# Performance work log

Hardware: AMD Instinct MI355X
Metric: run time of the kernel (lower is better)

## Reference

```python
import jax, jax.numpy as jnp
import numpy as np

N, D, B, P, T = 2048, 64, 64, 16384, 262144
EPS = 1e-6        # const.eps in the original repo
LAST_TIME = 1.0   # init_time = 0


def setup_inputs() -> dict:
    key = jax.random.key(0)
    k = jax.random.split(key, 8)
    x0 = jax.random.normal(k[0], (N, D), dtype=jnp.float32)
    v = 0.1 * jax.random.normal(k[1], (B, N, D), dtype=jnp.float32)
    beta = jax.random.normal(k[2], (N,), dtype=jnp.float32)
    bins_rwidth = jax.random.normal(k[3], (B,), dtype=jnp.float32)
    # distinct node pairs (i != j) to avoid degenerate zero-distance pairs
    i = jax.random.randint(k[4], (P,), 0, N, dtype=jnp.int32)
    off = jax.random.randint(k[5], (P,), 1, N, dtype=jnp.int32)
    node_pairs = jnp.stack([i, (i + off) % N], axis=0)  # [2, P]
    event_times = jax.random.uniform(k[6], (T,), dtype=jnp.float32) * LAST_TIME
    event_pair_idx = jax.random.randint(k[7], (T,), 0, P, dtype=jnp.int32)
    return {"x0": x0, "v": v, "beta": beta, "bins_rwidth": bins_rwidth,
            "event_times": event_times, "node_pairs": node_pairs,
            "event_pair_idx": event_pair_idx}


def reference(x0, v, beta, bins_rwidth, event_times, node_pairs, event_pair_idx):
    # bin bounds: softmax(relative widths) -> cumsum over the timeline
    bounds = jnp.concatenate([jnp.zeros((1,), x0.dtype),
                              jnp.cumsum(jax.nn.softmax(bins_rwidth)) * LAST_TIME])  # [B+1]
    widths = bounds[1:] - bounds[:-1]          # [B]
    inner = bounds[1:-1]                       # bucketize boundaries

    i, j = node_pairs[0], node_pairs[1]
    dx0 = x0[i] - x0[j]                        # [P, D]
    dv = v[:, i, :] - v[:, j, :]               # [B, P, D]
    # cumulative displacement at each bin boundary
    cum = jnp.concatenate([jnp.zeros((1, dx0.shape[0], dx0.shape[1]), dx0.dtype),
                           jnp.cumsum(dv * widths[:, None, None], axis=0)], axis=0)  # [B+1, P, D]
    beta_sum = beta[i] + beta[j]               # [P]

    # ---- intensity integral over the bin bounds (closed form per bin) ----
    idx_b = jnp.searchsorted(inner, bounds, side='right')          # torch.bucketize right=True
    rem_b = bounds - bounds[idx_b]
    xt_b = dx0[None] + cum[idx_b] + dv[idx_b] * rem_b[:, None, None]  # [B+1, P, D]
    norm_b = jnp.linalg.norm(xt_b, axis=2)                         # [B+1, P]
    numer = norm_b * jnp.exp(beta_sum[None, :] - norm_b)
    dot1 = jnp.sum(xt_b[1:] * dv, axis=2)                          # [B, P]
    dot0 = jnp.sum(xt_b[:-1] * dv, axis=2)
    integral = jnp.sum(numer[1:] / (dot1 + EPS) - numer[:-1] / (dot0 + EPS))

    # ---- ragged event log-intensities (flattened: events -> pair ids) ----
    idx_e = jnp.searchsorted(inner, event_times, side='right')     # [T]
    rem_e = event_times - bounds[idx_e]
    pid = event_pair_idx
    xt_e = dx0[pid] + cum[idx_e, pid] + dv[idx_e, pid] * rem_e[:, None]  # [T, D]
    dist_e = jnp.linalg.norm(xt_e, axis=1)
    non_integral = jnp.sum(beta_sum[pid] - dist_e)

    # NLL = -(-integral + non_integral)
    return integral - non_integral
```

## Files before the change

### kernel.cpp

```cpp
#include <hip/hip_runtime.h>

#define NN 2048
#define DD 64
#define BB 64
#define PP 16384
#define TT 262144
#define EPSF 1e-6f
#define SS ((size_t)NN * DD)


typedef unsigned uv2 __attribute__((ext_vector_type(2)));
using bf16x8 = __attribute__((ext_vector_type(8))) short;
using f32x4v = __attribute__((ext_vector_type(4))) float;

template <int CTRL, int RM = 0xF, bool BC = true>
__device__ __forceinline__ float dpp_add(float x) {
    int y = __builtin_amdgcn_update_dpp(0, __float_as_int(x), CTRL, RM, 0xF, BC);
    return x + __int_as_float(y);
}

template <int PAT>
__device__ __forceinline__ float swz_add(float x) {
    return x + __int_as_float(__builtin_amdgcn_ds_swizzle(__float_as_int(x), PAT));
}

__device__ __forceinline__ float xor16_add(float x) {
#if __has_builtin(__builtin_amdgcn_permlane16_swap)
    uv2 r = __builtin_amdgcn_permlane16_swap(__float_as_uint(x), __float_as_uint(x),
                                             false, false);
    return __uint_as_float(r.x) + __uint_as_float(r.y);
#else
    return swz_add<0x401F>(x);
#endif
}
__device__ __forceinline__ float xor32_add(float x) {
#if __has_builtin(__builtin_amdgcn_permlane32_swap)
    uv2 r = __builtin_amdgcn_permlane32_swap(__float_as_uint(x), __float_as_uint(x),
                                             false, false);
    return __uint_as_float(r.x) + __uint_as_float(r.y);
#else
    return x + __shfl_xor(x, 32, 64);
#endif
}

__device__ __forceinline__ float reduce1(float a) {
    a = dpp_add<0xB1>(a);
    a = dpp_add<0x4E>(a);
    a = dpp_add<0x141>(a);
    a = swz_add<0x201F>(a);
    a = xor16_add(a);
    a = xor32_add(a);
    return a;
}

__device__ __forceinline__ float incl_scan(float x) {
    x = dpp_add<0x111>(x);
    x = dpp_add<0x112>(x);
    x = dpp_add<0x114>(x);
    x = dpp_add<0x118>(x);
    x = dpp_add<0x142, 0xA, false>(x);
    x = dpp_add<0x143, 0xC, false>(x);
    return x;
}

__device__ __forceinline__ unsigned short f2bf(float f) {
    unsigned u = __float_as_uint(f);
    unsigned r = (u + 0x7FFFu + ((u >> 16) & 1u)) >> 16;
    return (unsigned short)r;
}
__device__ __forceinline__ float bf_lo(unsigned u) { return __uint_as_float(u << 16); }
__device__ __forceinline__ float bf_hi(unsigned u) { return __uint_as_float(u & 0xFFFF0000u); }

__device__ __forceinline__ unsigned cvt_pk_bf(float lo, float hi) {
    unsigned r;
    asm("v_cvt_pk_bf16_f32 %0, %1, %2" : "=v"(r) : "v"(lo), "v"(hi));
    return r;
}
__device__ __forceinline__ float bpermf(float v, int srclane) {
    return __int_as_float(__builtin_amdgcn_ds_bpermute(srclane << 2, __float_as_int(v)));
}

__global__ void k_bounds(const float* __restrict__ brw, float* __restrict__ bounds,
                         float* __restrict__ widths, float* __restrict__ innerPad,
                         int* __restrict__ cnt, double* __restrict__ acc) {
    if (blockIdx.x != 0) {
        int t = (blockIdx.x - 1) * 64 + threadIdx.x;
#pragma unroll
        for (int k = 0; k < 4; k++) cnt[t * 4 + k] = 0;
        if (blockIdx.x == 1 && threadIdx.x == 0) acc[0] = 0.0;
        return;
    }
    int lane = threadIdx.x;
    float w = brw[lane];
    float m = w;
#pragma unroll
    for (int s = 32; s >= 1; s >>= 1) m = fmaxf(m, __shfl_xor(m, s, 64));
    float e = expf(w - m);
    float tot = e;
#pragma unroll
    for (int s = 32; s >= 1; s >>= 1) tot += __shfl_xor(tot, s, 64);
    float sm = e / tot;
    float c = sm;
#pragma unroll
    for (int off = 1; off < 64; off <<= 1) {
        float t = __shfl_up(c, off, 64);
        if (lane >= off) c += t;
    }
    float cexcl = __shfl_up(c, 1, 64);
    if (lane == 0) cexcl = 0.f;
    if (lane == 0) bounds[0] = 0.f;
    bounds[lane + 1] = c;
    widths[lane] = c - cexcl;
    innerPad[lane] = (lane == 63) ? 3.4e38f : c;
}

__global__ __launch_bounds__(256) void k_convert(const float* __restrict__ v,
                                                 unsigned* __restrict__ vh32) {
    int wid = threadIdx.x >> 6, lane = threadIdx.x & 63;
    int n = blockIdx.x * 4 + wid;
    int sub = lane >> 5;
    int dp = (lane & 31) * 2;
    unsigned* __restrict__ dst = vh32 + ((size_t)n * BB * DD) / 2;
#pragma unroll
    for (int c = 0; c < 32; c++) {
        int b = c * 2 + sub;
        float2 f = *(const float2*)(v + (size_t)b * SS + (size_t)n * DD + dp);
        unsigned pk = (unsigned)f2bf(f.x) | ((unsigned)f2bf(f.y) << 16);
        dst[(b * DD + dp) / 2] = pk;
    }
}

__global__ void k_hist2(const int* __restrict__ pairs, int* __restrict__ cnt) {
    int t = blockIdx.x * 256 + threadIdx.x;
    atomicAdd(&cnt[pairs[t]], 1);
}

__global__ __launch_bounds__(1024) void k_scan2(const int* __restrict__ cnt,
                                                int* __restrict__ cursor) {
    __shared__ int waveTot[16];
    __shared__ int waveOff[16];
    int tid = threadIdx.x;
    int a = cnt[tid * 2], b = cnt[tid * 2 + 1];
    int s = a + b;
    int lane = tid & 63, wid = tid >> 6;
    int incl = s;
#pragma unroll
    for (int off = 1; off < 64; off <<= 1) {
        int t2 = __shfl_up(incl, off, 64);
        if (lane >= off) incl += t2;
    }
    if (lane == 63) waveTot[wid] = incl;
    __syncthreads();
    if (tid == 0) {
        int r = 0;
        for (int w = 0; w < 16; w++) { waveOff[w] = r; r += waveTot[w]; }
    }
    __syncthreads();
    int run = waveOff[wid] + (incl - s);
    cursor[tid * 2] = run;
    cursor[tid * 2 + 1] = run + a;
}

__global__ void k_scatter2(const int* __restrict__ pairs, int* __restrict__ cursor,
                           int* __restrict__ perm) {
    int t = blockIdx.x * 256 + threadIdx.x;
    int pos = atomicAdd(&cursor[pairs[t]], 1);
    perm[pos] = t;
}

__global__ __launch_bounds__(256, 2) void k_pairs(
    const float* __restrict__ x0, const uint4* __restrict__ vh4,
    const float* __restrict__ beta, const int* __restrict__ pairs,
    const int* __restrict__ perm, const float* __restrict__ widths,
    float4* __restrict__ table, double* __restrict__ acc_out) {
    __shared__ double bacc[4];
    const int wid = threadIdx.x >> 6;
    const int lane = threadIdx.x & 63;
    const int bid = blockIdx.x;
    const int vb = ((bid & 7) << 7) | (bid >> 3);
    const int pbase = (vb * 4 + wid) * 4;

    int pk[4], ik[4], jk[4];
    float bs[4];
#pragma unroll
    for (int k = 0; k < 4; k++) pk[k] = perm[pbase + k];
#pragma unroll
    for (int k = 0; k < 4; k++) {
        ik[k] = pairs[pk[k]];
        jk[k] = pairs[PP + pk[k]];
    }
#pragma unroll
    for (int k = 0; k < 4; k++) bs[k] = beta[ik[k]] + beta[jk[k]];

    float wv[4][4];
#pragma unroll
    for (int tm = 0; tm < 4; tm++)
#pragma unroll
        for (int r = 0; r < 4; r++)
            wv[tm][r] = widths[16 * tm + (lane >> 4) * 4 + r];
    const float wl = widths[lane];
    const int laneterm = (lane & 15) * 8 + (lane >> 4);
    const int nl = lane & 15;
    const int mb = (lane >> 4) * 4;

    uint4 ra[8], rb[8];
    float xiv, xjv;

#define ISSUE(k_)                                                            \
    {                                                                        \
        const uint4* Vi = vh4 + (size_t)ik[k_] * 512 + laneterm;             \
        const uint4* Vj = vh4 + (size_t)jk[k_] * 512 + laneterm;             \
        _Pragma("unroll") for (int t = 0; t < 4; t++) {                      \
            ra[t * 2 + 0] = Vi[t * 128];                                     \
            ra[t * 2 + 1] = Vi[t * 128 + 4];                                 \
            rb[t * 2 + 0] = Vj[t * 128];                                     \
            rb[t * 2 + 1] = Vj[t * 128 + 4];                                 \
        }                                                                    \
        xiv = x0[ik[k_] * DD + lane];                                        \
        xjv = x0[jk[k_] * DD + lane];                                        \
    }

    ISSUE(0)

    double accd = 0.0;

#pragma unroll
    for (int k = 0; k < 4; k++) {
        const float bsum = bs[k];
        float dx0 = xiv - xjv;
        float n2_0 = reduce1(dx0 * dx0);
        float rr0 = __builtin_amdgcn_sqrtf(n2_0);
        float numer0 = rr0 * __expf(bsum - rr0);

        bf16x8 F[8];
#pragma unroll
        for (int f = 0; f < 8; f++) {
            uint4 q;
            q.x = cvt_pk_bf(bf_lo(ra[f].x) - bf_lo(rb[f].x), bf_hi(ra[f].x) - bf_hi(rb[f].x));
            q.y = cvt_pk_bf(bf_lo(ra[f].y) - bf_lo(rb[f].y), bf_hi(ra[f].y) - bf_hi(rb[f].y));
            q.z = cvt_pk_bf(bf_lo(ra[f].z) - bf_lo(rb[f].z), bf_hi(ra[f].z) - bf_hi(rb[f].z));
            q.w = cvt_pk_bf(bf_lo(ra[f].w) - bf_lo(rb[f].w), bf_hi(ra[f].w) - bf_hi(rb[f].w));
            union { uint4 u; bf16x8 s; } cv;
            cv.u = q;
            F[f] = cv.s;
        }

        if (k < 3) {
            if (k == 0) ISSUE(1)
            if (k == 1) ISSUE(2)
            if (k == 2) ISSUE(3)
        }

        bf16x8 AX[2];
#pragma unroll
        for (int kb = 0; kb < 2; kb++) {
            unsigned u[4];
#pragma unroll
            for (int c2 = 0; c2 < 4; c2++) {
                int k0 = kb * 32 + ((lane >> 4) << 3) + c2 * 2;
                u[c2] = cvt_pk_bf(bpermf(dx0, k0), bpermf(dx0, k0 + 1));
            }
            uint4 q;
            bool z = (lane & 15) != 0;
            q.x = z ? 0u : u[0]; q.y = z ? 0u : u[1];
            q.z = z ? 0u : u[2]; q.w = z ? 0u : u[3];
            union { uint4 uu; bf16x8 s; } cv;
            cv.uu = q;
            AX[kb] = cv.s;
        }

        f32x4v g00 = {0.f, 0.f, 0.f, 0.f}, g01 = g00, g02 = g00, g03 = g00;
        f32x4v g11 = g00, g12 = g00, g13 = g00, g22 = g00, g23 = g00, g33 = g00;
#define GMM(acc, ta, tb)                                                                       \
    acc = __builtin_amdgcn_mfma_f32_16x16x32_bf16(F[(ta)*2 + 0], F[(tb)*2 + 0], acc, 0, 0, 0); \
    acc = __builtin_amdgcn_mfma_f32_16x16x32_bf16(F[(ta)*2 + 1], F[(tb)*2 + 1], acc, 0, 0, 0);
        GMM(g00, 0, 0) GMM(g01, 0, 1) GMM(g02, 0, 2) GMM(g03, 0, 3)
        GMM(g11, 1, 1) GMM(g12, 1, 2) GMM(g13, 1, 3)
        GMM(g22, 2, 2) GMM(g23, 2, 3) GMM(g33, 3, 3)
#undef GMM
        float c00, c01, c02, c03;
        {
            f32x4v ca = {0.f, 0.f, 0.f, 0.f};
#define CMM(tb)                                                                        \
    ca = __builtin_amdgcn_mfma_f32_16x16x32_bf16(AX[0], F[(tb)*2 + 0], ca, 0, 0, 0);  \
    ca = __builtin_amdgcn_mfma_f32_16x16x32_bf16(AX[1], F[(tb)*2 + 1], ca, 0, 0, 0);
            CMM(0) c00 = ca[0]; ca = {0.f, 0.f, 0.f, 0.f};
            CMM(1) c01 = ca[0]; ca = {0.f, 0.f, 0.f, 0.f};
            CMM(2) c02 = ca[0]; ca = {0.f, 0.f, 0.f, 0.f};
            CMM(3) c03 = ca[0];
#undef CMM
        }

        float c0v;
        {
            float b0 = bpermf(c00, lane & 15);
            float b1 = bpermf(c01, lane & 15);
            float b2 = bpermf(c02, lane & 15);
            float b3 = bpermf(c03, lane & 15);
            int g = lane >> 4;
            c0v = (g == 0) ? b0 : (g == 1) ? b1 : (g == 2) ? b2 : b3;
        }

        float Sv = 0.f, qv = 0.f;
#define OFFT(gt, t_) (wv[t_][0] * gt[0] + wv[t_][1] * gt[1] + wv[t_][2] * gt[2] + wv[t_][3] * gt[3])
#define DIAG(d, t_)                                       \
    sp += (mb + 0 < nl) ? wv[t_][0] * d[0] : 0.f;         \
    sp += (mb + 1 < nl) ? wv[t_][1] * d[1] : 0.f;         \
    sp += (mb + 2 < nl) ? wv[t_][2] * d[2] : 0.f;         \
    sp += (mb + 3 < nl) ? wv[t_][3] * d[3] : 0.f;         \
    qp += (mb + 0 == nl) ? d[0] : 0.f;                    \
    qp += (mb + 1 == nl) ? d[1] : 0.f;                    \
    qp += (mb + 2 == nl) ? d[2] : 0.f;                    \
    qp += (mb + 3 == nl) ? d[3] : 0.f;
#define FINTN(t_)                                         \
    sp = xor16_add(sp); sp = xor32_add(sp);               \
    qp = xor16_add(qp); qp = xor32_add(qp);               \
    if ((lane >> 4) == t_) { Sv = sp; qv = qp; }
        {
            float sp = 0.f, qp = 0.f;
            DIAG(g00, 0) FINTN(0)
        }
        {
            float sp = OFFT(g01, 0), qp = 0.f;
            DIAG(g11, 1) FINTN(1)
        }
        {
            float sp = OFFT(g02, 0) + OFFT(g12, 1), qp = 0.f;
            DIAG(g22, 2) FINTN(2)
        }
        {
            float sp = OFFT(g03, 0) + OFFT(g13, 1) + OFFT(g23, 2), qp = 0.f;
            DIAG(g33, 3) FINTN(3)
        }
#undef OFFT
#undef DIAG
#undef FINTN

        float d0r = c0v + Sv;
        float qqr = qv;

        float tt = wl * fmaf(wl, qqr, 2.f * d0r);
        float incl = incl_scan(tt);
        float n2L = fmaxf(n2_0 + (incl - tt), 0.f);
        float n2R = fmaxf(n2_0 + incl, 0.f);
        float rrR = __builtin_amdgcn_sqrtf(n2R);
        float numerR = rrR * __expf(bsum - rrR);
        float numerL = __int_as_float(
            __builtin_amdgcn_update_dpp(0, __float_as_int(numerR), 0x138, 0xF, 0xF, true));
        numerL = (lane == 0) ? numer0 : numerL;
        float pd = fmaf(wl, qqr, d0r);
        float term = numerR * __builtin_amdgcn_rcpf(pd + EPSF)
                   - numerL * __builtin_amdgcn_rcpf(d0r + EPSF);
        float acc = reduce1(term);

        table[(size_t)pk[k] * BB + lane] = make_float4(n2L, d0r, qqr, bsum);
        accd += (double)acc;
    }
#undef ISSUE

    if (lane == 0) bacc[wid] = accd;
    __syncthreads();
    if (threadIdx.x == 0)
        atomicAdd(acc_out, bacc[0] + bacc[1] + bacc[2] + bacc[3]);
}

__global__ __launch_bounds__(256) void k_events(
    const float* __restrict__ times, const int* __restrict__ epid,
    const float* __restrict__ bounds, const float* __restrict__ innerPad,
    const float4* __restrict__ table, double* __restrict__ acc_out) {
    __shared__ float si[64];
    __shared__ float sb[BB + 1];
    __shared__ double wacc[4];
    int tid = threadIdx.x;
    if (tid < 64) si[tid] = innerPad[tid];
    if (tid <= BB) sb[tid] = bounds[tid];
    __syncthreads();
    int g = (blockIdx.x * 256 + tid) * 2;
    float2 tm2 = *(const float2*)(times + g);
    int2 pd2 = *(const int2*)(epid + g);
    float tms[2] = {tm2.x, tm2.y};
    int pids[2] = {pd2.x, pd2.y};
    int cc[2];
    float rem[2];
#pragma unroll
    for (int k = 0; k < 2; k++) {
        int c = 0;
        float tm = tms[k];
#pragma unroll
        for (int s = 32; s >= 1; s >>= 1)
            if (si[c + s - 1] <= tm) c += s;
        cc[k] = c;
        rem[k] = tm - sb[c];
    }
    float4 e0 = table[(size_t)pids[0] * BB + cc[0]];
    float4 e1 = table[(size_t)pids[1] * BB + cc[1]];
    float eacc;
    {
        float d2 = fmaxf(fmaf(rem[0], fmaf(rem[0], e0.z, 2.f * e0.y), e0.x), 0.f);
        eacc = e0.w - __builtin_amdgcn_sqrtf(d2);
        d2 = fmaxf(fmaf(rem[1], fmaf(rem[1], e1.z, 2.f * e1.y), e1.x), 0.f);
        eacc += e1.w - __builtin_amdgcn_sqrtf(d2);
    }
    float val = reduce1(eacc);
    if ((tid & 63) == 0) wacc[tid >> 6] = (double)val;
    __syncthreads();
    if (tid == 0)
        atomicAdd(acc_out, -(wacc[0] + wacc[1] + wacc[2] + wacc[3]));
}

__global__ void k_finalize(const double* __restrict__ acc, float* __restrict__ out) {
    out[0] = (float)(*acc);
}

extern "C" void kernel_launch(void* const* d_in, const int* in_sizes, int n_in,
                              void* d_out, int out_size, void* d_ws, size_t ws_size,
                              hipStream_t stream) {
    const float* x0     = (const float*)d_in[0];
    const float* v      = (const float*)d_in[1];
    const float* beta   = (const float*)d_in[2];
    const float* brw    = (const float*)d_in[3];
    const float* etimes = (const float*)d_in[4];
    const int*   pairs  = (const int*)d_in[5];
    const int*   epid   = (const int*)d_in[6];

    char* ws = (char*)d_ws;
    double* acc     = (double*)ws;
    int* cnt        = (int*)(ws + 1024);
    int* cursor     = (int*)(ws + 9216);
    int* perm       = (int*)(ws + 17408);
    float* bounds   = (float*)(ws + 82944);
    float* widths   = (float*)(ws + 83456);
    float* innerPad = (float*)(ws + 83968);
    float4* table   = (float4*)(ws + 84480);
    unsigned* vh32  = (unsigned*)(ws + 84480 + (size_t)PP * BB * 16);

    hipLaunchKernelGGL(k_bounds, dim3(9), dim3(64), 0, stream, brw, bounds, widths,
                       innerPad, cnt, acc);
    hipLaunchKernelGGL(k_convert, dim3(NN / 4), dim3(256), 0, stream, v, vh32);
    hipLaunchKernelGGL(k_hist2, dim3(PP / 256), dim3(256), 0, stream, pairs, cnt);
    hipLaunchKernelGGL(k_scan2, dim3(1), dim3(1024), 0, stream, cnt, cursor);
    hipLaunchKernelGGL(k_scatter2, dim3(PP / 256), dim3(256), 0, stream, pairs, cursor, perm);
    hipLaunchKernelGGL(k_pairs, dim3(PP / 16), dim3(256), 0, stream, x0, (const uint4*)vh32,
                       beta, pairs, perm, widths, table, acc);
    hipLaunchKernelGGL(k_events, dim3(TT / 512), dim3(256), 0, stream, etimes, epid,
                       bounds, innerPad, table, acc);
    hipLaunchKernelGGL(k_finalize, dim3(1), dim3(1), 0, stream, acc, (float*)d_out);
}
```

Measured before the change: 78.74 us.

## Double-buffer pair loads over 8 pairs per wave and fuse histogram into convert

```diff
diff --git a/kernel.cpp b/kernel.cpp
--- a/kernel.cpp
+++ b/kernel.cpp
@@ -114,8 +114,15 @@
     innerPad[lane] = (lane == 63) ? 3.4e38f : c;
 }
 
-__global__ __launch_bounds__(256) void k_convert(const float* __restrict__ v,
-                                                 unsigned* __restrict__ vh32) {
+__global__ __launch_bounds__(256) void k_convert_hist(const float* __restrict__ v,
+                                                      unsigned* __restrict__ vh32,
+                                                      const int* __restrict__ pairs,
+                                                      int* __restrict__ cnt) {
+    if (blockIdx.x >= NN / 4) {
+        int t = (blockIdx.x - NN / 4) * 256 + threadIdx.x;
+        atomicAdd(&cnt[pairs[t]], 1);
+        return;
+    }
     int wid = threadIdx.x >> 6, lane = threadIdx.x & 63;
     int n = blockIdx.x * 4 + wid;
     int sub = lane >> 5;
@@ -128,11 +135,6 @@
         unsigned pk = (unsigned)f2bf(f.x) | ((unsigned)f2bf(f.y) << 16);
         dst[(b * DD + dp) / 2] = pk;
     }
-}
-
-__global__ void k_hist2(const int* __restrict__ pairs, int* __restrict__ cnt) {
-    int t = blockIdx.x * 256 + threadIdx.x;
-    atomicAdd(&cnt[pairs[t]], 1);
 }
 
 __global__ __launch_bounds__(1024) void k_scan2(const int* __restrict__ cnt,
@@ -177,20 +179,20 @@
     const int wid = threadIdx.x >> 6;
     const int lane = threadIdx.x & 63;
     const int bid = blockIdx.x;
-    const int vb = ((bid & 7) << 7) | (bid >> 3);
-    const int pbase = (vb * 4 + wid) * 4;
-
-    int pk[4], ik[4], jk[4];
-    float bs[4];
-#pragma unroll
-    for (int k = 0; k < 4; k++) pk[k] = perm[pbase + k];
-#pragma unroll
-    for (int k = 0; k < 4; k++) {
+    const int vb = ((bid & 7) << 6) | (bid >> 3);
+    const int pbase = (vb * 4 + wid) * 8;
+
+    int pk[8], ik[8], jk[8];
+    float bs[8];
+#pragma unroll
+    for (int k = 0; k < 8; k++) pk[k] = perm[pbase + k];
+#pragma unroll
+    for (int k = 0; k < 8; k++) {
         ik[k] = pairs[pk[k]];
         jk[k] = pairs[PP + pk[k]];
     }
 #pragma unroll
-    for (int k = 0; k < 4; k++) bs[k] = beta[ik[k]] + beta[jk[k]];
+    for (int k = 0; k < 8; k++) bs[k] = beta[ik[k]] + beta[jk[k]];
 
     float wv[4][4];
 #pragma unroll
@@ -203,105 +205,112 @@
     const int nl = lane & 15;
     const int mb = (lane >> 4) * 4;
 
-    uint4 ra[8], rb[8];
-    float xiv, xjv;
-
-#define ISSUE(k_)                                                            \
+    uint4 ra0[8], rb0[8], ra1[8], rb1[8];
+    float xi0, xj0, xi1, xj1;
+
+#define ISSUE(RA, RB, XI, XJ, k_)                                            \
     {                                                                        \
         const uint4* Vi = vh4 + (size_t)ik[k_] * 512 + laneterm;             \
         const uint4* Vj = vh4 + (size_t)jk[k_] * 512 + laneterm;             \
         _Pragma("unroll") for (int t = 0; t < 4; t++) {                      \
-            ra[t * 2 + 0] = Vi[t * 128];                                     \
-            ra[t * 2 + 1] = Vi[t * 128 + 4];                                 \
-            rb[t * 2 + 0] = Vj[t * 128];                                     \
-            rb[t * 2 + 1] = Vj[t * 128 + 4];                                 \
+            RA[t * 2 + 0] = Vi[t * 128];                                     \
+            RA[t * 2 + 1] = Vi[t * 128 + 4];                                 \
+            RB[t * 2 + 0] = Vj[t * 128];                                     \
+            RB[t * 2 + 1] = Vj[t * 128 + 4];                                 \
         }                                                                    \
-        xiv = x0[ik[k_] * DD + lane];                                        \
-        xjv = x0[jk[k_] * DD + lane];                                        \
-    }
-
-    ISSUE(0)
+        XI = x0[ik[k_] * DD + lane];                                         \
+        XJ = x0[jk[k_] * DD + lane];                                         \
+    }
 
     double accd = 0.0;
 
-#pragma unroll
-    for (int k = 0; k < 4; k++) {
-        const float bsum = bs[k];
-        float dx0 = xiv - xjv;
-        float n2_0 = reduce1(dx0 * dx0);
-        float rr0 = __builtin_amdgcn_sqrtf(n2_0);
-        float numer0 = rr0 * __expf(bsum - rr0);
-
-        bf16x8 F[8];
-#pragma unroll
-        for (int f = 0; f < 8; f++) {
-            uint4 q;
-            q.x = cvt_pk_bf(bf_lo(ra[f].x) - bf_lo(rb[f].x), bf_hi(ra[f].x) - bf_hi(rb[f].x));
-            q.y = cvt_pk_bf(bf_lo(ra[f].y) - bf_lo(rb[f].y), bf_hi(ra[f].y) - bf_hi(rb[f].y));
-            q.z = cvt_pk_bf(bf_lo(ra[f].z) - bf_lo(rb[f].z), bf_hi(ra[f].z) - bf_hi(rb[f].z));
-            q.w = cvt_pk_bf(bf_lo(ra[f].w) - bf_lo(rb[f].w), bf_hi(ra[f].w) - bf_hi(rb[f].w));
-            union { uint4 u; bf16x8 s; } cv;
-            cv.u = q;
-            F[f] = cv.s;
-        }
-
-        if (k < 3) {
-            if (k == 0) ISSUE(1)
-            if (k == 1) ISSUE(2)
-            if (k == 2) ISSUE(3)
-        }
-
-        bf16x8 AX[2];
-#pragma unroll
-        for (int kb = 0; kb < 2; kb++) {
-            unsigned u[4];
-#pragma unroll
-            for (int c2 = 0; c2 < 4; c2++) {
-                int k0 = kb * 32 + ((lane >> 4) << 3) + c2 * 2;
-                u[c2] = cvt_pk_bf(bpermf(dx0, k0), bpermf(dx0, k0 + 1));
-            }
-            uint4 q;
-            bool z = (lane & 15) != 0;
-            q.x = z ? 0u : u[0]; q.y = z ? 0u : u[1];
-            q.z = z ? 0u : u[2]; q.w = z ? 0u : u[3];
-            union { uint4 uu; bf16x8 s; } cv;
-            cv.uu = q;
-            AX[kb] = cv.s;
-        }
-
-        f32x4v g00 = {0.f, 0.f, 0.f, 0.f}, g01 = g00, g02 = g00, g03 = g00;
-        f32x4v g11 = g00, g12 = g00, g13 = g00, g22 = g00, g23 = g00, g33 = g00;
+#define STEP(RA, RB, XI, XJ, k_, NEXTISSUE)                                                    \
+    {                                                                                          \
+        const float bsum = bs[k_];                                                             \
+        float dx0 = XI - XJ;                                                                   \
+        float n2_0 = reduce1(dx0 * dx0);                                                       \
+        float rr0 = __builtin_amdgcn_sqrtf(n2_0);                                              \
+        float numer0 = rr0 * __expf(bsum - rr0);                                               \
+        bf16x8 F[8];                                                                           \
+        _Pragma("unroll") for (int f = 0; f < 8; f++) {                                        \
+            uint4 q;                                                                           \
+            q.x = cvt_pk_bf(bf_lo(RA[f].x) - bf_lo(RB[f].x), bf_hi(RA[f].x) - bf_hi(RB[f].x)); \
+            q.y = cvt_pk_bf(bf_lo(RA[f].y) - bf_lo(RB[f].y), bf_hi(RA[f].y) - bf_hi(RB[f].y)); \
+            q.z = cvt_pk_bf(bf_lo(RA[f].z) - bf_lo(RB[f].z), bf_hi(RA[f].z) - bf_hi(RB[f].z)); \
+            q.w = cvt_pk_bf(bf_lo(RA[f].w) - bf_lo(RB[f].w), bf_hi(RA[f].w) - bf_hi(RB[f].w)); \
+            union { uint4 u; bf16x8 s; } cv;                                                   \
+            cv.u = q;                                                                          \
+            F[f] = cv.s;                                                                       \
+        }                                                                                      \
+        NEXTISSUE                                                                              \
+        bf16x8 AX[2];                                                                          \
+        _Pragma("unroll") for (int kb = 0; kb < 2; kb++) {                                     \
+            unsigned u[4];                                                                     \
+            _Pragma("unroll") for (int c2 = 0; c2 < 4; c2++) {                                 \
+                int k0 = kb * 32 + ((lane >> 4) << 3) + c2 * 2;                                \
+                u[c2] = cvt_pk_bf(bpermf(dx0, k0), bpermf(dx0, k0 + 1));                       \
+            }                                                                                  \
+            uint4 q;                                                                           \
+            bool z = (lane & 15) != 0;                                                         \
+            q.x = z ? 0u : u[0]; q.y = z ? 0u : u[1];                                          \
+            q.z = z ? 0u : u[2]; q.w = z ? 0u : u[3];                                          \
+            union { uint4 uu; bf16x8 s; } cv;                                                  \
+            cv.uu = q;                                                                         \
+            AX[kb] = cv.s;                                                                     \
+        }                                                                                      \
+        f32x4v g00 = {0.f, 0.f, 0.f, 0.f}, g01 = g00, g02 = g00, g03 = g00;                    \
+        f32x4v g11 = g00, g12 = g00, g13 = g00, g22 = g00, g23 = g00, g33 = g00;               \
+        GMM(g00, 0, 0) GMM(g01, 0, 1) GMM(g02, 0, 2) GMM(g03, 0, 3)                            \
+        GMM(g11, 1, 1) GMM(g12, 1, 2) GMM(g13, 1, 3)                                           \
+        GMM(g22, 2, 2) GMM(g23, 2, 3) GMM(g33, 3, 3)                                           \
+        float c00, c01, c02, c03;                                                              \
+        {                                                                                      \
+            f32x4v ca = {0.f, 0.f, 0.f, 0.f};                                                  \
+            CMM(0) c00 = ca[0]; ca = {0.f, 0.f, 0.f, 0.f};                                     \
+            CMM(1) c01 = ca[0]; ca = {0.f, 0.f, 0.f, 0.f};                                     \
+            CMM(2) c02 = ca[0]; ca = {0.f, 0.f, 0.f, 0.f};                                     \
+            CMM(3) c03 = ca[0];                                                                \
+        }                                                                                      \
+        float c0v;                                                                             \
+        {                                                                                      \
+            float b0 = bpermf(c00, lane & 15);                                                 \
+            float b1 = bpermf(c01, lane & 15);                                                 \
+            float b2 = bpermf(c02, lane & 15);                                                 \
+            float b3 = bpermf(c03, lane & 15);                                                 \
+            int g = lane >> 4;                                                                 \
+            c0v = (g == 0) ? b0 : (g == 1) ? b1 : (g == 2) ? b2 : b3;                          \
+        }                                                                                      \
+        float Sv = 0.f, qv = 0.f;                                                              \
+        { float sp = 0.f, qp = 0.f;                                 DIAG(g00, 0) FINTN(0) }    \
+        { float sp = OFFT(g01, 0), qp = 0.f;                        DIAG(g11, 1) FINTN(1) }    \
+        { float sp = OFFT(g02, 0) + OFFT(g12, 1), qp = 0.f;         DIAG(g22, 2) FINTN(2) }    \
+        { float sp = OFFT(g03, 0) + OFFT(g13, 1) + OFFT(g23, 2), qp = 0.f;                     \
+                                                                    DIAG(g33, 3) FINTN(3) }    \
+        float d0r = c0v + Sv;                                                                  \
+        float qqr = qv;                                                                        \
+        float tt = wl * fmaf(wl, qqr, 2.f * d0r);                                              \
+        float incl = incl_scan(tt);                                                            \
+        float n2L = fmaxf(n2_0 + (incl - tt), 0.f);                                            \
+        float n2R = fmaxf(n2_0 + incl, 0.f);                                                   \
+        float rrR = __builtin_amdgcn_sqrtf(n2R);                                               \
+        float numerR = rrR * __expf(bsum - rrR);                                               \
+        float numerL = __int_as_float(                                                         \
+            __builtin_amdgcn_update_dpp(0, __float_as_int(numerR), 0x138, 0xF, 0xF, true));    \
+        numerL = (lane == 0) ? numer0 : numerL;                                                \
+        float pd = fmaf(wl, qqr, d0r);                                                         \
+        float term = numerR * __builtin_amdgcn_rcpf(pd + EPSF)                                 \
+                   - numerL * __builtin_amdgcn_rcpf(d0r + EPSF);                               \
+        float acc = reduce1(term);                                                             \
+        table[(size_t)pk[k_] * BB + lane] = make_float4(n2L, d0r, qqr, bsum);                  \
+        accd += (double)acc;                                                                   \
+    }
+
 #define GMM(acc, ta, tb)                                                                       \
     acc = __builtin_amdgcn_mfma_f32_16x16x32_bf16(F[(ta)*2 + 0], F[(tb)*2 + 0], acc, 0, 0, 0); \
     acc = __builtin_amdgcn_mfma_f32_16x16x32_bf16(F[(ta)*2 + 1], F[(tb)*2 + 1], acc, 0, 0, 0);
-        GMM(g00, 0, 0) GMM(g01, 0, 1) GMM(g02, 0, 2) GMM(g03, 0, 3)
-        GMM(g11, 1, 1) GMM(g12, 1, 2) GMM(g13, 1, 3)
-        GMM(g22, 2, 2) GMM(g23, 2, 3) GMM(g33, 3, 3)
-#undef GMM
-        float c00, c01, c02, c03;
-        {
-            f32x4v ca = {0.f, 0.f, 0.f, 0.f};
-#define CMM(tb)                                                                        \
-    ca = __builtin_amdgcn_mfma_f32_16x16x32_bf16(AX[0], F[(tb)*2 + 0], ca, 0, 0, 0);  \
+#define CMM(tb)                                                                       \
+    ca = __builtin_amdgcn_mfma_f32_16x16x32_bf16(AX[0], F[(tb)*2 + 0], ca, 0, 0, 0); \
     ca = __builtin_amdgcn_mfma_f32_16x16x32_bf16(AX[1], F[(tb)*2 + 1], ca, 0, 0, 0);
-            CMM(0) c00 = ca[0]; ca = {0.f, 0.f, 0.f, 0.f};
-            CMM(1) c01 = ca[0]; ca = {0.f, 0.f, 0.f, 0.f};
-            CMM(2) c02 = ca[0]; ca = {0.f, 0.f, 0.f, 0.f};
-            CMM(3) c03 = ca[0];
-#undef CMM
-        }
-
-        float c0v;
-        {
-            float b0 = bpermf(c00, lane & 15);
-            float b1 = bpermf(c01, lane & 15);
-            float b2 = bpermf(c02, lane & 15);
-            float b3 = bpermf(c03, lane & 15);
-            int g = lane >> 4;
-            c0v = (g == 0) ? b0 : (g == 1) ? b1 : (g == 2) ? b2 : b3;
-        }
-
-        float Sv = 0.f, qv = 0.f;
 #define OFFT(gt, t_) (wv[t_][0] * gt[0] + wv[t_][1] * gt[1] + wv[t_][2] * gt[2] + wv[t_][3] * gt[3])
 #define DIAG(d, t_)                                       \
     sp += (mb + 0 < nl) ? wv[t_][0] * d[0] : 0.f;         \
@@ -316,47 +325,26 @@
     sp = xor16_add(sp); sp = xor32_add(sp);               \
     qp = xor16_add(qp); qp = xor32_add(qp);               \
     if ((lane >> 4) == t_) { Sv = sp; qv = qp; }
-        {
-            float sp = 0.f, qp = 0.f;
-            DIAG(g00, 0) FINTN(0)
-        }
-        {
-            float sp = OFFT(g01, 0), qp = 0.f;
-            DIAG(g11, 1) FINTN(1)
-        }
-        {
-            float sp = OFFT(g02, 0) + OFFT(g12, 1), qp = 0.f;
-            DIAG(g22, 2) FINTN(2)
-        }
-        {
-            float sp = OFFT(g03, 0) + OFFT(g13, 1) + OFFT(g23, 2), qp = 0.f;
-            DIAG(g33, 3) FINTN(3)
-        }
+
+    ISSUE(ra0, rb0, xi0, xj0, 0)
+    ISSUE(ra1, rb1, xi1, xj1, 1)
+
+    STEP(ra0, rb0, xi0, xj0, 0, ISSUE(ra0, rb0, xi0, xj0, 2))
+    STEP(ra1, rb1, xi1, xj1, 1, ISSUE(ra1, rb1, xi1, xj1, 3))
+    STEP(ra0, rb0, xi0, xj0, 2, ISSUE(ra0, rb0, xi0, xj0, 4))
+    STEP(ra1, rb1, xi1, xj1, 3, ISSUE(ra1, rb1, xi1, xj1, 5))
+    STEP(ra0, rb0, xi0, xj0, 4, ISSUE(ra0, rb0, xi0, xj0, 6))
+    STEP(ra1, rb1, xi1, xj1, 5, ISSUE(ra1, rb1, xi1, xj1, 7))
+    STEP(ra0, rb0, xi0, xj0, 6, )
+    STEP(ra1, rb1, xi1, xj1, 7, )
+
+#undef ISSUE
+#undef STEP
+#undef GMM
+#undef CMM
 #undef OFFT
 #undef DIAG
 #undef FINTN
-
-        float d0r = c0v + Sv;
-        float qqr = qv;
-
-        float tt = wl * fmaf(wl, qqr, 2.f * d0r);
-        float incl = incl_scan(tt);
-        float n2L = fmaxf(n2_0 + (incl - tt), 0.f);
-        float n2R = fmaxf(n2_0 + incl, 0.f);
-        float rrR = __builtin_amdgcn_sqrtf(n2R);
-        float numerR = rrR * __expf(bsum - rrR);
-        float numerL = __int_as_float(
-            __builtin_amdgcn_update_dpp(0, __float_as_int(numerR), 0x138, 0xF, 0xF, true));
-        numerL = (lane == 0) ? numer0 : numerL;
-        float pd = fmaf(wl, qqr, d0r);
-        float term = numerR * __builtin_amdgcn_rcpf(pd + EPSF)
-                   - numerL * __builtin_amdgcn_rcpf(d0r + EPSF);
-        float acc = reduce1(term);
-
-        table[(size_t)pk[k] * BB + lane] = make_float4(n2L, d0r, qqr, bsum);
-        accd += (double)acc;
-    }
-#undef ISSUE
 
     if (lane == 0) bacc[wid] = accd;
     __syncthreads();
@@ -436,11 +424,11 @@
 
     hipLaunchKernelGGL(k_bounds, dim3(9), dim3(64), 0, stream, brw, bounds, widths,
                        innerPad, cnt, acc);
-    hipLaunchKernelGGL(k_convert, dim3(NN / 4), dim3(256), 0, stream, v, vh32);
-    hipLaunchKernelGGL(k_hist2, dim3(PP / 256), dim3(256), 0, stream, pairs, cnt);
+    hipLaunchKernelGGL(k_convert_hist, dim3(NN / 4 + PP / 256), dim3(256), 0, stream,
+                       v, vh32, pairs, cnt);
     hipLaunchKernelGGL(k_scan2, dim3(1), dim3(1024), 0, stream, cnt, cursor);
     hipLaunchKernelGGL(k_scatter2, dim3(PP / 256), dim3(256), 0, stream, pairs, cursor, perm);
-    hipLaunchKernelGGL(k_pairs, dim3(PP / 16), dim3(256), 0, stream, x0, (const uint4*)vh32,
+    hipLaunchKernelGGL(k_pairs, dim3(PP / 32), dim3(256), 0, stream, x0, (const uint4*)vh32,
                        beta, pairs, perm, widths, table, acc);
     hipLaunchKernelGGL(k_events, dim3(TT / 512), dim3(256), 0, stream, etimes, epid,
                        bounds, innerPad, table, acc);
```

Result: faster. 76.86 us (-2.4%).

## Fuse preprocessing kernels, reuse shared i-node loads, fold finalize into events

Applied to the files above, without the earlier changes.

```diff
diff --git a/kernel.cpp b/kernel.cpp
--- a/kernel.cpp
+++ b/kernel.cpp
@@ -10,6 +10,8 @@
 
 
 typedef unsigned uv2 __attribute__((ext_vector_type(2)));
+typedef float fx4 __attribute__((ext_vector_type(4)));
+typedef unsigned ux4 __attribute__((ext_vector_type(4)));
 using bf16x8 = __attribute__((ext_vector_type(8))) short;
 using f32x4v = __attribute__((ext_vector_type(4))) float;
 
@@ -63,10 +65,9 @@
     return x;
 }
 
-__device__ __forceinline__ unsigned short f2bf(float f) {
+__device__ __forceinline__ unsigned f2bf(float f) {
     unsigned u = __float_as_uint(f);
-    unsigned r = (u + 0x7FFFu + ((u >> 16) & 1u)) >> 16;
-    return (unsigned short)r;
+    return (u + 0x7FFFu + ((u >> 16) & 1u)) >> 16;
 }
 __device__ __forceinline__ float bf_lo(unsigned u) { return __uint_as_float(u << 16); }
 __device__ __forceinline__ float bf_hi(unsigned u) { return __uint_as_float(u & 0xFFFF0000u); }
@@ -80,68 +81,73 @@
     return __int_as_float(__builtin_amdgcn_ds_bpermute(srclane << 2, __float_as_int(v)));
 }
 
-__global__ void k_bounds(const float* __restrict__ brw, float* __restrict__ bounds,
-                         float* __restrict__ widths, float* __restrict__ innerPad,
-                         int* __restrict__ cnt, double* __restrict__ acc) {
-    if (blockIdx.x != 0) {
-        int t = (blockIdx.x - 1) * 64 + threadIdx.x;
-#pragma unroll
-        for (int k = 0; k < 4; k++) cnt[t * 4 + k] = 0;
-        if (blockIdx.x == 1 && threadIdx.x == 0) acc[0] = 0.0;
-        return;
-    }
-    int lane = threadIdx.x;
-    float w = brw[lane];
-    float m = w;
-#pragma unroll
-    for (int s = 32; s >= 1; s >>= 1) m = fmaxf(m, __shfl_xor(m, s, 64));
-    float e = expf(w - m);
-    float tot = e;
-#pragma unroll
-    for (int s = 32; s >= 1; s >>= 1) tot += __shfl_xor(tot, s, 64);
-    float sm = e / tot;
-    float c = sm;
-#pragma unroll
-    for (int off = 1; off < 64; off <<= 1) {
-        float t = __shfl_up(c, off, 64);
-        if (lane >= off) c += t;
-    }
-    float cexcl = __shfl_up(c, 1, 64);
-    if (lane == 0) cexcl = 0.f;
-    if (lane == 0) bounds[0] = 0.f;
-    bounds[lane + 1] = c;
-    widths[lane] = c - cexcl;
-    innerPad[lane] = (lane == 63) ? 3.4e38f : c;
-}
-
-__global__ __launch_bounds__(256) void k_convert(const float* __restrict__ v,
-                                                 unsigned* __restrict__ vh32) {
-    int wid = threadIdx.x >> 6, lane = threadIdx.x & 63;
-    int n = blockIdx.x * 4 + wid;
-    int sub = lane >> 5;
-    int dp = (lane & 31) * 2;
-    unsigned* __restrict__ dst = vh32 + ((size_t)n * BB * DD) / 2;
-#pragma unroll
-    for (int c = 0; c < 32; c++) {
-        int b = c * 2 + sub;
-        float2 f = *(const float2*)(v + (size_t)b * SS + (size_t)n * DD + dp);
-        unsigned pk = (unsigned)f2bf(f.x) | ((unsigned)f2bf(f.y) << 16);
-        dst[(b * DD + dp) / 2] = pk;
-    }
-}
-
-__global__ void k_hist2(const int* __restrict__ pairs, int* __restrict__ cnt) {
-    int t = blockIdx.x * 256 + threadIdx.x;
-    atomicAdd(&cnt[pairs[t]], 1);
-}
-
-__global__ __launch_bounds__(1024) void k_scan2(const int* __restrict__ cnt,
-                                                int* __restrict__ cursor) {
+__global__ __launch_bounds__(1024) void k_pre(
+    const float* __restrict__ v, unsigned* __restrict__ vh32,
+    const float* __restrict__ brw, float* __restrict__ bounds,
+    float* __restrict__ widths, float* __restrict__ innerPad,
+    const int* __restrict__ pairs, int* __restrict__ perm,
+    double* __restrict__ acc, int* __restrict__ done) {
+    __shared__ int scnt[2048];
     __shared__ int waveTot[16];
     __shared__ int waveOff[16];
-    int tid = threadIdx.x;
-    int a = cnt[tid * 2], b = cnt[tid * 2 + 1];
-    int s = a + b;
+    const int bid = blockIdx.x;
+    const int tid = threadIdx.x;
+
+    if (bid < 1024) {
+        const int bin = bid >> 4;
+        const int node0 = (bid & 15) << 7;
+        const fx4* __restrict__ src =
+            (const fx4*)(v + (size_t)bin * SS + (size_t)node0 * DD);
+        fx4 f0 = __builtin_nontemporal_load(src + tid * 2);
+        fx4 f1 = __builtin_nontemporal_load(src + tid * 2 + 1);
+        const int nn = tid >> 3;
+        const int d = (tid & 7) * 8;
+        ux4 o;
+        o.x = f2bf(f0.x) | (f2bf(f0.y) << 16);
+        o.y = f2bf(f0.z) | (f2bf(f0.w) << 16);
+        o.z = f2bf(f1.x) | (f2bf(f1.y) << 16);
+        o.w = f2bf(f1.z) | (f2bf(f1.w) << 16);
+        *(ux4*)(vh32 + (size_t)(node0 + nn) * 2048 + bin * 32 + d / 2) = o;
+        return;
+    }
+
+    if (bid == 1024) {
+        if (tid == 64) *acc = 0.0;
+        if (tid == 65) *done = 0;
+        if (tid >= 64) return;
+        int lane = tid;
+        float w = brw[lane];
+        float m = w;
+#pragma unroll
+        for (int s = 32; s >= 1; s >>= 1) m = fmaxf(m, __shfl_xor(m, s, 64));
+        float e = expf(w - m);
+        float tot = e;
+#pragma unroll
+        for (int s = 32; s >= 1; s >>= 1) tot += __shfl_xor(tot, s, 64);
+        float sm = e / tot;
+        float c = sm;
+#pragma unroll
+        for (int off = 1; off < 64; off <<= 1) {
+            float t = __shfl_up(c, off, 64);
+            if (lane >= off) c += t;
+        }
+        float cexcl = __shfl_up(c, 1, 64);
+        if (lane == 0) cexcl = 0.f;
+        if (lane == 0) bounds[0] = 0.f;
+        bounds[lane + 1] = c;
+        widths[lane] = c - cexcl;
+        innerPad[lane] = (lane == 63) ? 3.4e38f : c;
+        return;
+    }
+
+    scnt[tid] = 0;
+    scnt[tid + 1024] = 0;
+    __syncthreads();
+#pragma unroll
+    for (int k = 0; k < 16; k++) atomicAdd(&scnt[pairs[k * 1024 + tid]], 1);
+    __syncthreads();
+    int a = scnt[tid * 2], b2 = scnt[tid * 2 + 1];
+    int s = a + b2;
     int lane = tid & 63, wid = tid >> 6;
     int incl = s;
 #pragma unroll
@@ -157,15 +163,15 @@
     }
     __syncthreads();
     int run = waveOff[wid] + (incl - s);
-    cursor[tid * 2] = run;
-    cursor[tid * 2 + 1] = run + a;
-}
-
-__global__ void k_scatter2(const int* __restrict__ pairs, int* __restrict__ cursor,
-                           int* __restrict__ perm) {
-    int t = blockIdx.x * 256 + threadIdx.x;
-    int pos = atomicAdd(&cursor[pairs[t]], 1);
-    perm[pos] = t;
+    scnt[tid * 2] = run;
+    scnt[tid * 2 + 1] = run + a;
+    __syncthreads();
+#pragma unroll
+    for (int k = 0; k < 16; k++) {
+        int idx = k * 1024 + tid;
+        int pos = atomicAdd(&scnt[pairs[idx]], 1);
+        perm[pos] = idx;
+    }
 }
 
 __global__ __launch_bounds__(256, 2) void k_pairs(
@@ -177,20 +183,20 @@
     const int wid = threadIdx.x >> 6;
     const int lane = threadIdx.x & 63;
     const int bid = blockIdx.x;
-    const int vb = ((bid & 7) << 7) | (bid >> 3);
-    const int pbase = (vb * 4 + wid) * 4;
-
-    int pk[4], ik[4], jk[4];
-    float bs[4];
-#pragma unroll
-    for (int k = 0; k < 4; k++) pk[k] = perm[pbase + k];
-#pragma unroll
-    for (int k = 0; k < 4; k++) {
+    const int vb = ((bid & 7) << 6) | (bid >> 3);
+    const int pbase = (vb * 4 + wid) * 8;
+
+    int pk[8], ik[8], jk[8];
+    float bs[8];
+#pragma unroll
+    for (int k = 0; k < 8; k++) pk[k] = perm[pbase + k];
+#pragma unroll
+    for (int k = 0; k < 8; k++) {
         ik[k] = pairs[pk[k]];
         jk[k] = pairs[PP + pk[k]];
     }
 #pragma unroll
-    for (int k = 0; k < 4; k++) bs[k] = beta[ik[k]] + beta[jk[k]];
+    for (int k = 0; k < 8; k++) bs[k] = beta[ik[k]] + beta[jk[k]];
 
     float wv[4][4];
 #pragma unroll
@@ -203,105 +209,29 @@
     const int nl = lane & 15;
     const int mb = (lane >> 4) * 4;
 
-    uint4 ra[8], rb[8];
-    float xiv, xjv;
-
-#define ISSUE(k_)                                                            \
-    {                                                                        \
-        const uint4* Vi = vh4 + (size_t)ik[k_] * 512 + laneterm;             \
-        const uint4* Vj = vh4 + (size_t)jk[k_] * 512 + laneterm;             \
-        _Pragma("unroll") for (int t = 0; t < 4; t++) {                      \
-            ra[t * 2 + 0] = Vi[t * 128];                                     \
-            ra[t * 2 + 1] = Vi[t * 128 + 4];                                 \
-            rb[t * 2 + 0] = Vj[t * 128];                                     \
-            rb[t * 2 + 1] = Vj[t * 128 + 4];                                 \
-        }                                                                    \
-        xiv = x0[ik[k_] * DD + lane];                                        \
-        xjv = x0[jk[k_] * DD + lane];                                        \
-    }
-
-    ISSUE(0)
+    uint4 RA[8], RB[8];
+    float xi, xj;
+    {
+        const uint4* Vi = vh4 + (size_t)ik[0] * 512 + laneterm;
+#pragma unroll
+        for (int t = 0; t < 4; t++) {
+            RA[t * 2 + 0] = Vi[t * 128];
+            RA[t * 2 + 1] = Vi[t * 128 + 4];
+        }
+        xi = x0[ik[0] * DD + lane];
+    }
+    {
+        const uint4* Vj = vh4 + (size_t)jk[0] * 512 + laneterm;
+#pragma unroll
+        for (int t = 0; t < 4; t++) {
+            RB[t * 2 + 0] = Vj[t * 128];
+            RB[t * 2 + 1] = Vj[t * 128 + 4];
+        }
+        xj = x0[jk[0] * DD + lane];
+    }
 
     double accd = 0.0;
 
-#pragma unroll
-    for (int k = 0; k < 4; k++) {
-        const float bsum = bs[k];
-        float dx0 = xiv - xjv;
-        float n2_0 = reduce1(dx0 * dx0);
-        float rr0 = __builtin_amdgcn_sqrtf(n2_0);
-        float numer0 = rr0 * __expf(bsum - rr0);
-
-        bf16x8 F[8];
-#pragma unroll
-        for (int f = 0; f < 8; f++) {
-            uint4 q;
-            q.x = cvt_pk_bf(bf_lo(ra[f].x) - bf_lo(rb[f].x), bf_hi(ra[f].x) - bf_hi(rb[f].x));
-            q.y = cvt_pk_bf(bf_lo(ra[f].y) - bf_lo(rb[f].y), bf_hi(ra[f].y) - bf_hi(rb[f].y));
-            q.z = cvt_pk_bf(bf_lo(ra[f].z) - bf_lo(rb[f].z), bf_hi(ra[f].z) - bf_hi(rb[f].z));
-            q.w = cvt_pk_bf(bf_lo(ra[f].w) - bf_lo(rb[f].w), bf_hi(ra[f].w) - bf_hi(rb[f].w));
-            union { uint4 u; bf16x8 s; } cv;
-            cv.u = q;
-            F[f] = cv.s;
-        }
-
-        if (k < 3) {
-            if (k == 0) ISSUE(1)
-            if (k == 1) ISSUE(2)
-            if (k == 2) ISSUE(3)
-        }
-
-        bf16x8 AX[2];
-#pragma unroll
-        for (int kb = 0; kb < 2; kb++) {
-            unsigned u[4];
-#pragma unroll
-            for (int c2 = 0; c2 < 4; c2++) {
-                int k0 = kb * 32 + ((lane >> 4) << 3) + c2 * 2;
-                u[c2] = cvt_pk_bf(bpermf(dx0, k0), bpermf(dx0, k0 + 1));
-            }
-            uint4 q;
-            bool z = (lane & 15) != 0;
-            q.x = z ? 0u : u[0]; q.y = z ? 0u : u[1];
-            q.z = z ? 0u : u[2]; q.w = z ? 0u : u[3];
-            union { uint4 uu; bf16x8 s; } cv;
-            cv.uu = q;
-            AX[kb] = cv.s;
-        }
-
-        f32x4v g00 = {0.f, 0.f, 0.f, 0.f}, g01 = g00, g02 = g00, g03 = g00;
-        f32x4v g11 = g00, g12 = g00, g13 = g00, g22 = g00, g23 = g00, g33 = g00;
-#define GMM(acc, ta, tb)                                                                       \
-    acc = __builtin_amdgcn_mfma_f32_16x16x32_bf16(F[(ta)*2 + 0], F[(tb)*2 + 0], acc, 0, 0, 0); \
-    acc = __builtin_amdgcn_mfma_f32_16x16x32_bf16(F[(ta)*2 + 1], F[(tb)*2 + 1], acc, 0, 0, 0);
-        GMM(g00, 0, 0) GMM(g01, 0, 1) GMM(g02, 0, 2) GMM(g03, 0, 3)
-        GMM(g11, 1, 1) GMM(g12, 1, 2) GMM(g13, 1, 3)
-        GMM(g22, 2, 2) GMM(g23, 2, 3) GMM(g33, 3, 3)
-#undef GMM
-        float c00, c01, c02, c03;
-        {
-            f32x4v ca = {0.f, 0.f, 0.f, 0.f};
-#define CMM(tb)                                                                        \
-    ca = __builtin_amdgcn_mfma_f32_16x16x32_bf16(AX[0], F[(tb)*2 + 0], ca, 0, 0, 0);  \
-    ca = __builtin_amdgcn_mfma_f32_16x16x32_bf16(AX[1], F[(tb)*2 + 1], ca, 0, 0, 0);
-            CMM(0) c00 = ca[0]; ca = {0.f, 0.f, 0.f, 0.f};
-            CMM(1) c01 = ca[0]; ca = {0.f, 0.f, 0.f, 0.f};
-            CMM(2) c02 = ca[0]; ca = {0.f, 0.f, 0.f, 0.f};
-            CMM(3) c03 = ca[0];
-#undef CMM
-        }
-
-        float c0v;
-        {
-            float b0 = bpermf(c00, lane & 15);
-            float b1 = bpermf(c01, lane & 15);
-            float b2 = bpermf(c02, lane & 15);
-            float b3 = bpermf(c03, lane & 15);
-            int g = lane >> 4;
-            c0v = (g == 0) ? b0 : (g == 1) ? b1 : (g == 2) ? b2 : b3;
-        }
-
-        float Sv = 0.f, qv = 0.f;
 #define OFFT(gt, t_) (wv[t_][0] * gt[0] + wv[t_][1] * gt[1] + wv[t_][2] * gt[2] + wv[t_][3] * gt[3])
 #define DIAG(d, t_)                                       \
     sp += (mb + 0 < nl) ? wv[t_][0] * d[0] : 0.f;         \
@@ -316,26 +246,102 @@
     sp = xor16_add(sp); sp = xor32_add(sp);               \
     qp = xor16_add(qp); qp = xor32_add(qp);               \
     if ((lane >> 4) == t_) { Sv = sp; qv = qp; }
+#define GMM(acc, ta, tb)                                                                       \
+    acc = __builtin_amdgcn_mfma_f32_16x16x32_bf16(F[(ta)*2 + 0], F[(tb)*2 + 0], acc, 0, 0, 0); \
+    acc = __builtin_amdgcn_mfma_f32_16x16x32_bf16(F[(ta)*2 + 1], F[(tb)*2 + 1], acc, 0, 0, 0);
+#define CMM(tb)                                                                       \
+    ca = __builtin_amdgcn_mfma_f32_16x16x32_bf16(AX[0], F[(tb)*2 + 0], ca, 0, 0, 0); \
+    ca = __builtin_amdgcn_mfma_f32_16x16x32_bf16(AX[1], F[(tb)*2 + 1], ca, 0, 0, 0);
+
+#pragma unroll
+    for (int k = 0; k < 8; k++) {
+        const float bsum = bs[k];
+        float dx0 = xi - xj;
+        float n2_0 = reduce1(dx0 * dx0);
+        float rr0 = __builtin_amdgcn_sqrtf(n2_0);
+        float numer0 = rr0 * __expf(bsum - rr0);
+
+        bf16x8 F[8];
+#pragma unroll
+        for (int f = 0; f < 8; f++) {
+            uint4 q;
+            q.x = cvt_pk_bf(bf_lo(RA[f].x) - bf_lo(RB[f].x), bf_hi(RA[f].x) - bf_hi(RB[f].x));
+            q.y = cvt_pk_bf(bf_lo(RA[f].y) - bf_lo(RB[f].y), bf_hi(RA[f].y) - bf_hi(RB[f].y));
+            q.z = cvt_pk_bf(bf_lo(RA[f].z) - bf_lo(RB[f].z), bf_hi(RA[f].z) - bf_hi(RB[f].z));
+            q.w = cvt_pk_bf(bf_lo(RA[f].w) - bf_lo(RB[f].w), bf_hi(RA[f].w) - bf_hi(RB[f].w));
+            union { uint4 u; bf16x8 s; } cv;
+            cv.u = q;
+            F[f] = cv.s;
+        }
+
+        if (k < 7) {
+            if (__builtin_amdgcn_readfirstlane(ik[k + 1]) !=
+                __builtin_amdgcn_readfirstlane(ik[k])) {
+                const uint4* Vi = vh4 + (size_t)ik[k + 1] * 512 + laneterm;
+#pragma unroll
+                for (int t = 0; t < 4; t++) {
+                    RA[t * 2 + 0] = Vi[t * 128];
+                    RA[t * 2 + 1] = Vi[t * 128 + 4];
+                }
+                xi = x0[ik[k + 1] * DD + lane];
+            }
+            const uint4* Vj = vh4 + (size_t)jk[k + 1] * 512 + laneterm;
+#pragma unroll
+            for (int t = 0; t < 4; t++) {
+                RB[t * 2 + 0] = Vj[t * 128];
+                RB[t * 2 + 1] = Vj[t * 128 + 4];
+            }
+            xj = x0[jk[k + 1] * DD + lane];
+        }
+
+        bf16x8 AX[2];
+#pragma unroll
+        for (int kb = 0; kb < 2; kb++) {
+            unsigned u[4];
+#pragma unroll
+            for (int c2 = 0; c2 < 4; c2++) {
+                int k0 = kb * 32 + ((lane >> 4) << 3) + c2 * 2;
+                u[c2] = cvt_pk_bf(bpermf(dx0, k0), bpermf(dx0, k0 + 1));
+            }
+            uint4 q;
+            bool z = (lane & 15) != 0;
+            q.x = z ? 0u : u[0]; q.y = z ? 0u : u[1];
+            q.z = z ? 0u : u[2]; q.w = z ? 0u : u[3];
+            union { uint4 uu; bf16x8 s; } cv;
+            cv.uu = q;
+            AX[kb] = cv.s;
+        }
+
+        f32x4v g00 = {0.f, 0.f, 0.f, 0.f}, g01 = g00, g02 = g00, g03 = g00;
+        f32x4v g11 = g00, g12 = g00, g13 = g00, g22 = g00, g23 = g00, g33 = g00;
+        GMM(g00, 0, 0) GMM(g01, 0, 1) GMM(g02, 0, 2) GMM(g03, 0, 3)
+        GMM(g11, 1, 1) GMM(g12, 1, 2) GMM(g13, 1, 3)
+        GMM(g22, 2, 2) GMM(g23, 2, 3) GMM(g33, 3, 3)
+        float c00, c01, c02, c03;
         {
-            float sp = 0.f, qp = 0.f;
-            DIAG(g00, 0) FINTN(0)
-        }
+            f32x4v ca = {0.f, 0.f, 0.f, 0.f};
+            CMM(0) c00 = ca[0]; ca = {0.f, 0.f, 0.f, 0.f};
+            CMM(1) c01 = ca[0]; ca = {0.f, 0.f, 0.f, 0.f};
+            CMM(2) c02 = ca[0]; ca = {0.f, 0.f, 0.f, 0.f};
+            CMM(3) c03 = ca[0];
+        }
+
+        float c0v;
         {
-            float sp = OFFT(g01, 0), qp = 0.f;
-            DIAG(g11, 1) FINTN(1)
-        }
-        {
-            float sp = OFFT(g02, 0) + OFFT(g12, 1), qp = 0.f;
-            DIAG(g22, 2) FINTN(2)
-        }
-        {
-            float sp = OFFT(g03, 0) + OFFT(g13, 1) + OFFT(g23, 2), qp = 0.f;
-            DIAG(g33, 3) FINTN(3)
-        }
-#undef OFFT
-#undef DIAG
-#undef FINTN
-
+            float b0 = bpermf(c00, lane & 15);
+            float b1 = bpermf(c01, lane & 15);
+            float b2 = bpermf(c02, lane & 15);
+            float b3 = bpermf(c03, lane & 15);
+            int g = lane >> 4;
+            c0v = (g == 0) ? b0 : (g == 1) ? b1 : (g == 2) ? b2 : b3;
+        }
+
+        float Sv = 0.f, qv = 0.f;
+        { float sp = 0.f, qp = 0.f;                                 DIAG(g00, 0) FINTN(0) }
+        { float sp = OFFT(g01, 0), qp = 0.f;                        DIAG(g11, 1) FINTN(1) }
+        { float sp = OFFT(g02, 0) + OFFT(g12, 1), qp = 0.f;         DIAG(g22, 2) FINTN(2) }
+        { float sp = OFFT(g03, 0) + OFFT(g13, 1) + OFFT(g23, 2), qp = 0.f;
+                                                                    DIAG(g33, 3) FINTN(3) }
         float d0r = c0v + Sv;
         float qqr = qv;
 
@@ -356,7 +362,12 @@
         table[(size_t)pk[k] * BB + lane] = make_float4(n2L, d0r, qqr, bsum);
         accd += (double)acc;
     }
-#undef ISSUE
+
+#undef OFFT
+#undef DIAG
+#undef FINTN
+#undef GMM
+#undef CMM
 
     if (lane == 0) bacc[wid] = accd;
     __syncthreads();
@@ -367,7 +378,8 @@
 __global__ __launch_bounds__(256) void k_events(
     const float* __restrict__ times, const int* __restrict__ epid,
     const float* __restrict__ bounds, const float* __restrict__ innerPad,
-    const float4* __restrict__ table, double* __restrict__ acc_out) {
+    const float4* __restrict__ table, double* __restrict__ acc_out,
+    int* __restrict__ done, float* __restrict__ out) {
     __shared__ float si[64];
     __shared__ float sb[BB + 1];
     __shared__ double wacc[4];
@@ -404,12 +416,15 @@
     float val = reduce1(eacc);
     if ((tid & 63) == 0) wacc[tid >> 6] = (double)val;
     __syncthreads();
-    if (tid == 0)
+    if (tid == 0) {
         atomicAdd(acc_out, -(wacc[0] + wacc[1] + wacc[2] + wacc[3]));
-}
-
-__global__ void k_finalize(const double* __restrict__ acc, float* __restrict__ out) {
-    out[0] = (float)(*acc);
+        __threadfence();
+        int c = atomicAdd(done, 1);
+        if (c == (int)gridDim.x - 1) {
+            double a = atomicAdd(acc_out, 0.0);
+            out[0] = (float)a;
+        }
+    }
 }
 
 extern "C" void kernel_launch(void* const* d_in, const int* in_sizes, int n_in,
@@ -425,8 +440,7 @@
 
     char* ws = (char*)d_ws;
     double* acc     = (double*)ws;
-    int* cnt        = (int*)(ws + 1024);
-    int* cursor     = (int*)(ws + 9216);
+    int* done       = (int*)(ws + 1024);
     int* perm       = (int*)(ws + 17408);
     float* bounds   = (float*)(ws + 82944);
     float* widths   = (float*)(ws + 83456);
@@ -434,15 +448,10 @@
     float4* table   = (float4*)(ws + 84480);
     unsigned* vh32  = (unsigned*)(ws + 84480 + (size_t)PP * BB * 16);
 
-    hipLaunchKernelGGL(k_bounds, dim3(9), dim3(64), 0, stream, brw, bounds, widths,
-                       innerPad, cnt, acc);
-    hipLaunchKernelGGL(k_convert, dim3(NN / 4), dim3(256), 0, stream, v, vh32);
-    hipLaunchKernelGGL(k_hist2, dim3(PP / 256), dim3(256), 0, stream, pairs, cnt);
-    hipLaunchKernelGGL(k_scan2, dim3(1), dim3(1024), 0, stream, cnt, cursor);
-    hipLaunchKernelGGL(k_scatter2, dim3(PP / 256), dim3(256), 0, stream, pairs, cursor, perm);
-    hipLaunchKernelGGL(k_pairs, dim3(PP / 16), dim3(256), 0, stream, x0, (const uint4*)vh32,
+    hipLaunchKernelGGL(k_pre, dim3(1026), dim3(1024), 0, stream, v, vh32, brw,
+                       bounds, widths, innerPad, pairs, perm, acc, done);
+    hipLaunchKernelGGL(k_pairs, dim3(PP / 32), dim3(256), 0, stream, x0, (const uint4*)vh32,
                        beta, pairs, perm, widths, table, acc);
     hipLaunchKernelGGL(k_events, dim3(TT / 512), dim3(256), 0, stream, etimes, epid,
-                       bounds, innerPad, table, acc);
-    hipLaunchKernelGGL(k_finalize, dim3(1), dim3(1), 0, stream, acc, (float*)d_out);
-}
+                       bounds, innerPad, table, acc, done, (float*)d_out);
+}
```

Result: faster. 74.80 us (median of 2 runs) (-5.0%).
